# Optimization experiments

Measured on AMD Instinct MI355X. Metric: run time of the kernel, lower is better.

## Reference

```python
import jax, jax.numpy as jnp
import numpy as np

D_MODEL = 512
D_PROJ = 32
N_CENT = 6
CORR_HIDDEN = max(D_MODEL // 16, 32)  # 32
LN_EPS = 1e-5
ALPHA_DIR = 5.0


def _layernorm(x, g, b):
    mu = x.mean(axis=-1, keepdims=True)
    var = jnp.mean((x - mu) ** 2, axis=-1, keepdims=True)
    return (x - mu) * jax.lax.rsqrt(var + LN_EPS) * g + b


def _l2norm(x, eps=1e-12):
    n = jnp.sqrt(jnp.sum(x * x, axis=-1, keepdims=True))
    return x / jnp.maximum(n, eps)


def setup_inputs() -> dict:
    key = jax.random.key(0)
    ks = jax.random.split(key, 8)
    B, N = 64, 1024
    x = jax.random.normal(ks[0], (B, N, D_MODEL), dtype=jnp.float32)
    s_in = 1.0 / np.sqrt(D_MODEL)
    proj_w = jax.random.uniform(ks[1], (D_PROJ, D_MODEL), jnp.float32, -s_in, s_in)
    proj_b = jax.random.uniform(ks[2], (D_PROJ,), jnp.float32, -s_in, s_in)
    ln_g = jnp.ones((D_PROJ,), jnp.float32)
    ln_b = jnp.zeros((D_PROJ,), jnp.float32)
    centroids = jax.random.uniform(ks[3], (N_CENT, D_PROJ), jnp.float32, -3.0, 3.0)
    s_c = 1.0 / np.sqrt(D_MODEL + D_PROJ)
    corr_in_w = jax.random.uniform(ks[4], (CORR_HIDDEN, D_MODEL + D_PROJ), jnp.float32, -s_c, s_c)
    corr_in_b = jax.random.uniform(ks[5], (CORR_HIDDEN,), jnp.float32, -s_c, s_c)
    # correction_out is zero-init in the module; use small random values so the
    # correction path is numerically exercised by the baseline.
    corr_out_w = jax.random.normal(ks[6], (D_MODEL, CORR_HIDDEN), jnp.float32) * 0.02
    corr_out_b = jax.random.normal(ks[7], (D_MODEL,), jnp.float32) * 0.02
    return {
        "x": x, "proj_w": proj_w, "proj_b": proj_b, "ln_g": ln_g, "ln_b": ln_b,
        "centroids": centroids,
        "corr_in_w": corr_in_w, "corr_in_b": corr_in_b,
        "corr_out_w": corr_out_w, "corr_out_b": corr_out_b,
        "gate_alpha": jnp.float32(0.0),
        "routing_log_temp": jnp.float32(1.6),
        "scale_evidence": jnp.float32(5.0),
    }


def reference(x, proj_w, proj_b, ln_g, ln_b, centroids, corr_in_w, corr_in_b,
              corr_out_w, corr_out_b, gate_alpha, routing_log_temp, scale_evidence):
    B, N, D = x.shape
    # per-variate RevIN-style normalization over the variate axis (dim=1), unbiased std
    rev_mean = x.mean(axis=1, keepdims=True)
    rev_var = jnp.sum((x - rev_mean) ** 2, axis=1, keepdims=True) / (N - 1)
    rev_std = jnp.sqrt(rev_var) + 1e-5
    x_norm = (x - rev_mean) / rev_std
    # geometric routing: proj -> LN -> cosine sim against centroids
    Q = _layernorm(jnp.einsum("bnd,pd->bnp", x_norm, proj_w) + proj_b, ln_g, ln_b)
    Q_n = _l2norm(Q)                      # [B,N,P]
    K_n = _l2norm(centroids)              # [K,P]
    sim_cos = jnp.einsum("bnp,kp->bnk", Q_n, K_n)
    soft_assign = jax.nn.softmax(sim_cos * jnp.exp(routing_log_temp), axis=-1)
    centroid_ctx = jnp.einsum("bnk,kp->bnp", soft_assign, centroids)
    # centroid-conditioned correction MLP (dropout is identity in eval)
    corr_input = jnp.concatenate([x_norm, centroid_ctx], axis=-1)  # [B,N,D+P]
    h = jax.nn.gelu(jnp.einsum("bnc,hc->bnh", corr_input, corr_in_w) + corr_in_b, approximate=False)
    correction = (jnp.einsum("bnh,dh->bnd", h, corr_out_w) + corr_out_b) * rev_std
    gate = jax.nn.sigmoid(gate_alpha)
    out = x + gate * correction
    # DST uncertainty (no-grad diagnostic)
    sim_ctrl = jax.lax.stop_gradient(sim_cos)
    dir_gate = jax.nn.softplus((sim_ctrl - sim_ctrl.mean(axis=-1, keepdims=True)) * ALPHA_DIR)
    s_ev = jax.nn.softplus(jax.lax.stop_gradient(scale_evidence))
    S_train = jnp.sum(dir_gate * s_ev + 1.0, axis=-1, keepdims=True)
    u_std = N_CENT / S_train
    # losses
    gram = K_n @ K_n.T
    ortho_loss = jnp.mean((gram - jnp.eye(N_CENT, dtype=x.dtype)) ** 2)
    avg_routing = soft_assign.mean(axis=(0, 1))
    latent_loss = jnp.mean((avg_routing - 1.0 / N_CENT) ** 2)
    return out, u_std, ortho_loss, latent_loss
```

## Files before the change

### kernel.cpp

```cpp
#include <hip/hip_runtime.h>
#include <cstdint>
#include <cstddef>

#define N_DIM 1024
#define D_DIM 512
#define M_DIM 65536
#define NC 6

typedef float f32x4 __attribute__((ext_vector_type(4)));
typedef __bf16 bf16x8 __attribute__((ext_vector_type(8)));

__device__ __forceinline__ float sp_f(float z) {
    return z > 20.f ? z : log1pf(expf(z));
}

__global__ void k_pack(const float* __restrict__ pw, const float* __restrict__ ciw,
                       const float* __restrict__ cow, const float* __restrict__ cent,
                       const float* __restrict__ ga, const float* __restrict__ rlt,
                       const float* __restrict__ sev,
                       __bf16* __restrict__ bpa, __bf16* __restrict__ bpl,
                       __bf16* __restrict__ w3p,
                       float* __restrict__ kn, float* __restrict__ cw,
                       float* __restrict__ scal, float* __restrict__ out_ortho) {
    __shared__ float skn[NC * 32];
    __shared__ float ssq[36];
    int bid = blockIdx.x, tid = threadIdx.x;
    if (bid < 128) {
        int i = bid * 256 + tid;
        int c = i >> 9, k = i & 511;
        float w = (c < 32) ? pw[c * 512 + k] : ciw[(c - 32) * 544 + k];
        __bf16 hi = (__bf16)w;
        bpa[i] = hi;
        if (c < 32) bpl[i] = (__bf16)(w - (float)hi);
    } else if (bid < 192) {
        int j = (bid - 128) * 256 + tid;
        w3p[j] = (__bf16)cow[j];
    } else if (bid == 192) {
        if (tid < 192) {
            int k = tid >> 5, h = tid & 31;
            float s = 0.f;
            for (int p = 0; p < 32; ++p) s += cent[k * 32 + p] * ciw[h * 544 + 512 + p];
            cw[k * 32 + h] = s;
        } else if (tid < 192 + NC) {
            int k = tid - 192;
            float s = 0.f;
            for (int p = 0; p < 32; ++p) { float v = cent[k * 32 + p]; s += v * v; }
            float inv = 1.f / fmaxf(sqrtf(s), 1e-12f);
            for (int p = 0; p < 32; ++p) kn[k * 32 + p] = cent[k * 32 + p] * inv;
        } else if (tid == 198) {
            scal[0] = expf(rlt[0]);
            scal[1] = sp_f(sev[0]);
            scal[2] = 1.f / (1.f + expf(-ga[0]));
        }
    } else {
        if (tid < NC) {
            float s = 0.f;
            for (int p = 0; p < 32; ++p) { float v = cent[tid * 32 + p]; s += v * v; }
            float inv = 1.f / fmaxf(sqrtf(s), 1e-12f);
            for (int p = 0; p < 32; ++p) skn[tid * 32 + p] = cent[tid * 32 + p] * inv;
        }
        __syncthreads();
        if (tid < 36) {
            int i = tid / 6, j = tid % 6;
            float g = 0.f;
            for (int p = 0; p < 32; ++p) g += skn[i * 32 + p] * skn[j * 32 + p];
            float d = g - (i == j ? 1.f : 0.f);
            ssq[tid] = d * d;
        }
        __syncthreads();
        if (tid == 0) {
            float s = 0.f;
            for (int i = 0; i < 36; ++i) s += ssq[i];
            *out_ortho = s / 36.f;
        }
    }
}

__global__ void k_stat1(const float* __restrict__ x, float* __restrict__ part) {
    int bid = blockIdx.x;
    int b = bid >> 5, sub = bid & 31;
    int d4 = threadIdx.x * 4;
    const float* px = x + ((size_t)(b * 1024 + sub * 32)) * 512 + d4;
    f32x4 s = {0.f, 0.f, 0.f, 0.f}, q = s;
    #pragma unroll 8
    for (int i = 0; i < 32; ++i) {
        float4 v = *(const float4*)(px + (size_t)i * 512);
        s.x += v.x; s.y += v.y; s.z += v.z; s.w += v.w;
        q.x += v.x * v.x; q.y += v.y * v.y; q.z += v.z * v.z; q.w += v.w * v.w;
    }
    *(f32x4*)(part + (size_t)bid * 512 + d4) = s;
    *(f32x4*)(part + (size_t)(2048 + bid) * 512 + d4) = q;
}

__global__ void k_stat2(const float* __restrict__ part, float* __restrict__ mean,
                        float* __restrict__ istd, float* __restrict__ stdv) {
    int b = blockIdx.x, d = threadIdx.x;
    float s = 0.f, q = 0.f;
    for (int c = 0; c < 32; ++c) {
        s += part[(size_t)(b * 32 + c) * 512 + d];
        q += part[(size_t)(2048 + b * 32 + c) * 512 + d];
    }
    float mu = s * (1.f / (float)N_DIM);
    float var = fmaxf((q - s * mu) * (1.f / (float)(N_DIM - 1)), 0.f);
    float sd = sqrtf(var) + 1e-5f;
    mean[b * D_DIM + d] = mu;
    istd[b * D_DIM + d] = 1.f / sd;
    stdv[b * D_DIM + d] = sd;
}

__launch_bounds__(256)
__global__ void mega(const float* __restrict__ x,
                     const float* __restrict__ proj_b, const float* __restrict__ ln_g,
                     const float* __restrict__ ln_b, const float* __restrict__ cib,
                     const float* __restrict__ cob,
                     const float* __restrict__ mean, const float* __restrict__ istd,
                     const float* __restrict__ stdv,
                     const float* __restrict__ kn, const float* __restrict__ cw,
                     const float* __restrict__ scal,
                     const __bf16* __restrict__ bpa, const __bf16* __restrict__ bpl,
                     const __bf16* __restrict__ w3p,
                     float* __restrict__ out, float* __restrict__ ustd_out,
                     float* __restrict__ rout_part) {
    __shared__ float s_mean[512];
    __shared__ float s_is[512];
    __shared__ float s_sd[512];
    __shared__ float s_cob[512];
    __shared__ __align__(16) float s_t[3][16][68];
    __shared__ __align__(16) __bf16 s_h[16][40];

    int tid = threadIdx.x;
    int wv = tid >> 6, ln = tid & 63;
    int l15 = ln & 15, lg = ln >> 4;

    int b = blockIdx.x >> 6;
    int wrow = blockIdx.x * 16;

    if (tid < 128) {
        *(float4*)&s_mean[tid * 4] = *(const float4*)(mean + b * 512 + tid * 4);
        *(float4*)&s_sd[tid * 4]   = *(const float4*)(stdv + b * 512 + tid * 4);
    } else {
        int t = tid - 128;
        *(float4*)&s_is[t * 4]  = *(const float4*)(istd + b * 512 + t * 4);
        *(float4*)&s_cob[t * 4] = *(const float4*)(cob + t * 4);
    }
    __syncthreads();

    int kbase = wv * 128;
    const float* xr = x + (size_t)(wrow + l15) * 512 + kbase;
    const __bf16* w0  = bpa + (size_t)l15 * 512 + kbase;
    const __bf16* w1  = bpa + (size_t)(16 + l15) * 512 + kbase;
    const __bf16* w2  = bpa + (size_t)(32 + l15) * 512 + kbase;
    const __bf16* w3  = bpa + (size_t)(48 + l15) * 512 + kbase;
    const __bf16* wl0 = bpl + (size_t)l15 * 512 + kbase;
    const __bf16* wl1 = bpl + (size_t)(16 + l15) * 512 + kbase;

    f32x4 a0 = {0.f, 0.f, 0.f, 0.f}, a1 = a0, a2 = a0, a3 = a0;
    #pragma unroll
    for (int ks = 0; ks < 4; ++ks) {
        int k0 = ks * 32 + lg * 8;
        int kk = kbase + k0;
        float4 xa = *(const float4*)(xr + k0);
        float4 xb = *(const float4*)(xr + k0 + 4);
        float4 ma = *(const float4*)&s_mean[kk];
        float4 m2 = *(const float4*)&s_mean[kk + 4];
        float4 ia = *(const float4*)&s_is[kk];
        float4 i2 = *(const float4*)&s_is[kk + 4];
        float xnf[8];
        xnf[0] = (xa.x - ma.x) * ia.x; xnf[1] = (xa.y - ma.y) * ia.y;
        xnf[2] = (xa.z - ma.z) * ia.z; xnf[3] = (xa.w - ma.w) * ia.w;
        xnf[4] = (xb.x - m2.x) * i2.x; xnf[5] = (xb.y - m2.y) * i2.y;
        xnf[6] = (xb.z - m2.z) * i2.z; xnf[7] = (xb.w - m2.w) * i2.w;
        bf16x8 ah, al;
        #pragma unroll
        for (int j = 0; j < 8; ++j) {
            __bf16 hh = (__bf16)xnf[j];
            ah[j] = hh;
            al[j] = (__bf16)(xnf[j] - (float)hh);
        }
        bf16x8 wh0 = *(const bf16x8*)(w0 + k0);
        bf16x8 wh1 = *(const bf16x8*)(w1 + k0);
        a0 = __builtin_amdgcn_mfma_f32_16x16x32_bf16(ah, wh0, a0, 0, 0, 0);
        a0 = __builtin_amdgcn_mfma_f32_16x16x32_bf16(ah, *(const bf16x8*)(wl0 + k0), a0, 0, 0, 0);
        a0 = __builtin_amdgcn_mfma_f32_16x16x32_bf16(al, wh0, a0, 0, 0, 0);
        a1 = __builtin_amdgcn_mfma_f32_16x16x32_bf16(ah, wh1, a1, 0, 0, 0);
        a1 = __builtin_amdgcn_mfma_f32_16x16x32_bf16(ah, *(const bf16x8*)(wl1 + k0), a1, 0, 0, 0);
        a1 = __builtin_amdgcn_mfma_f32_16x16x32_bf16(al, wh1, a1, 0, 0, 0);
        a2 = __builtin_amdgcn_mfma_f32_16x16x32_bf16(ah, *(const bf16x8*)(w2 + k0), a2, 0, 0, 0);
        a3 = __builtin_amdgcn_mfma_f32_16x16x32_bf16(ah, *(const bf16x8*)(w3 + k0), a3, 0, 0, 0);
    }

    if (wv != 0) {
        int j = wv - 1;
        #pragma unroll
        for (int rg = 0; rg < 4; ++rg) {
            int row = lg * 4 + rg;
            s_t[j][row][l15]      = a0[rg];
            s_t[j][row][16 + l15] = a1[rg];
            s_t[j][row][32 + l15] = a2[rg];
            s_t[j][row][48 + l15] = a3[rg];
        }
    }
    __syncthreads();

    if (wv == 0) {
        #pragma unroll
        for (int rg = 0; rg < 4; ++rg) {
            int row = lg * 4 + rg;
            a0[rg] += s_t[0][row][l15]      + s_t[1][row][l15]      + s_t[2][row][l15];
            a1[rg] += s_t[0][row][16 + l15] + s_t[1][row][16 + l15] + s_t[2][row][16 + l15];
            a2[rg] += s_t[0][row][32 + l15] + s_t[1][row][32 + l15] + s_t[2][row][32 + l15];
            a3[rg] += s_t[0][row][48 + l15] + s_t[1][row][48 + l15] + s_t[2][row][48 + l15];
            s_t[0][row][l15]      = a0[rg];
            s_t[0][row][16 + l15] = a1[rg];
            s_t[0][row][32 + l15] = a2[rg];
            s_t[0][row][48 + l15] = a3[rg];
        }

        int r = ln >> 2, sub = ln & 3;
        const float* tr = &s_t[0][r][0];
        float4 t0 = *(const float4*)(tr + sub * 8);
        float4 t1 = *(const float4*)(tr + sub * 8 + 4);
        float4 pb0 = *(const float4*)(proj_b + sub * 8);
        float4 pb1 = *(const float4*)(proj_b + sub * 8 + 4);
        float P[8];
        P[0] = t0.x + pb0.x; P[1] = t0.y + pb0.y; P[2] = t0.z + pb0.z; P[3] = t0.w + pb0.w;
        P[4] = t1.x + pb1.x; P[5] = t1.y + pb1.y; P[6] = t1.z + pb1.z; P[7] = t1.w + pb1.w;
        float m = 0.f;
        #pragma unroll
        for (int j = 0; j < 8; ++j) m += P[j];
        m += __shfl_xor(m, 1); m += __shfl_xor(m, 2);
        float mu = m * (1.f / 32.f);
        float v = 0.f;
        #pragma unroll
        for (int j = 0; j < 8; ++j) { float d = P[j] - mu; v += d * d; }
        v += __shfl_xor(v, 1); v += __shfl_xor(v, 2);
        float rs = rsqrtf(v * (1.f / 32.f) + 1e-5f);
        float4 g0 = *(const float4*)(ln_g + sub * 8);
        float4 g1 = *(const float4*)(ln_g + sub * 8 + 4);
        float4 bl0 = *(const float4*)(ln_b + sub * 8);
        float4 bl1 = *(const float4*)(ln_b + sub * 8 + 4);
        float gg[8] = {g0.x, g0.y, g0.z, g0.w, g1.x, g1.y, g1.z, g1.w};
        float bb[8] = {bl0.x, bl0.y, bl0.z, bl0.w, bl1.x, bl1.y, bl1.z, bl1.w};
        float q[8]; float n2 = 0.f;
        #pragma unroll
        for (int j = 0; j < 8; ++j) {
            q[j] = (P[j] - mu) * rs * gg[j] + bb[j];
            n2 += q[j] * q[j];
        }
        n2 += __shfl_xor(n2, 1); n2 += __shfl_xor(n2, 2);
        float inv = 1.f / fmaxf(sqrtf(n2), 1e-12f);
        float sim[6];
        #pragma unroll
        for (int k = 0; k < 6; ++k) {
            const float* kr = kn + k * 32 + sub * 8;
            float4 ka = *(const float4*)(kr);
            float4 kb = *(const float4*)(kr + 4);
            float s = q[0] * ka.x + q[1] * ka.y + q[2] * ka.z + q[3] * ka.w
                    + q[4] * kb.x + q[5] * kb.y + q[6] * kb.z + q[7] * kb.w;
            s += __shfl_xor(s, 1); s += __shfl_xor(s, 2);
            sim[k] = s * inv;
        }
        float T = scal[0], sevv = scal[1];
        float mx = sim[0];
        #pragma unroll
        for (int k = 1; k < 6; ++k) mx = fmaxf(mx, sim[k]);
        float e[6], es = 0.f;
        #pragma unroll
        for (int k = 0; k < 6; ++k) { e[k] = expf((sim[k] - mx) * T); es += e[k]; }
        float einv = 1.f / es;
        float a[6];
        #pragma unroll
        for (int k = 0; k < 6; ++k) a[k] = e[k] * einv;
        float msim = 0.f;
        #pragma unroll
        for (int k = 0; k < 6; ++k) msim += sim[k];
        msim *= (1.f / 6.f);
        float S = 6.f;
        #pragma unroll
        for (int k = 0; k < 6; ++k) S += sevv * sp_f((sim[k] - msim) * 5.f);
        if (sub == 0) ustd_out[wrow + r] = 6.f / S;
        float4 h0 = *(const float4*)(tr + 32 + sub * 8);
        float4 h1 = *(const float4*)(tr + 32 + sub * 8 + 4);
        float4 c0 = *(const float4*)(cib + sub * 8);
        float4 c1 = *(const float4*)(cib + sub * 8 + 4);
        float vh[8] = {h0.x + c0.x, h0.y + c0.y, h0.z + c0.z, h0.w + c0.w,
                       h1.x + c1.x, h1.y + c1.y, h1.z + c1.z, h1.w + c1.w};
        #pragma unroll
        for (int k = 0; k < 6; ++k) {
            const float* cr = cw + k * 32 + sub * 8;
            float4 ca = *(const float4*)(cr);
            float4 cb = *(const float4*)(cr + 4);
            vh[0] += a[k] * ca.x; vh[1] += a[k] * ca.y; vh[2] += a[k] * ca.z; vh[3] += a[k] * ca.w;
            vh[4] += a[k] * cb.x; vh[5] += a[k] * cb.y; vh[6] += a[k] * cb.z; vh[7] += a[k] * cb.w;
        }
        bf16x8 hv;
        #pragma unroll
        for (int j = 0; j < 8; ++j) {
            float gv = 0.5f * vh[j] * (1.f + erff(vh[j] * 0.70710678118654752f));
            hv[j] = (__bf16)gv;
        }
        *(bf16x8*)(&s_h[r][sub * 8]) = hv;
        #pragma unroll
        for (int k = 0; k < 6; ++k) {
            float rv = (sub == 0) ? a[k] : 0.f;
            rv += __shfl_xor(rv, 4); rv += __shfl_xor(rv, 8);
            rv += __shfl_xor(rv, 16); rv += __shfl_xor(rv, 32);
            if (ln == 0) atomicAdd(rout_part + (blockIdx.x & 63) * 6 + k, rv);
        }
    }
    __syncthreads();

    bf16x8 ha = *(const bf16x8*)(&s_h[l15][lg * 8]);
    float gate = scal[2];
    int row = wrow + l15;
    const float* xrow = x + (size_t)row * 512;
    float* orow = out + (size_t)row * 512;
    #pragma unroll
    for (int i = 0; i < 8; ++i) {
        int nf = wv * 8 + i;
        int col = nf * 16 + l15;
        bf16x8 wb = *(const bf16x8*)(w3p + col * 32 + lg * 8);
        f32x4 z = {0.f, 0.f, 0.f, 0.f};
        f32x4 d = __builtin_amdgcn_mfma_f32_16x16x32_bf16(wb, ha, z, 0, 0, 0);
        int colb = nf * 16 + lg * 4;
        float4 xv = *(const float4*)(xrow + colb);
        float4 bi = *(const float4*)&s_cob[colb];
        float4 sd = *(const float4*)&s_sd[colb];
        f32x4 o;
        o[0] = xv.x + gate * ((d[0] + bi.x) * sd.x);
        o[1] = xv.y + gate * ((d[1] + bi.y) * sd.y);
        o[2] = xv.z + gate * ((d[2] + bi.z) * sd.z);
        o[3] = xv.w + gate * ((d[3] + bi.w) * sd.w);
        *(f32x4*)(orow + colb) = o;
    }
}

__global__ void k5(const float* __restrict__ rp, float* __restrict__ out_latent) {
    __shared__ float sv[6];
    int t = threadIdx.x;
    if (t < 6) {
        float s = 0.f;
        for (int i = 0; i < 64; ++i) s += rp[i * 6 + t];
        sv[t] = s;
    }
    __syncthreads();
    if (t == 0) {
        float s = 0.f;
        for (int k = 0; k < 6; ++k) {
            float av = sv[k] * (1.f / (float)M_DIM) - (1.f / 6.f);
            s += av * av;
        }
        *out_latent = s / 6.f;
    }
}

extern "C" void kernel_launch(void* const* d_in, const int* in_sizes, int n_in,
                              void* d_out, int out_size, void* d_ws, size_t ws_size,
                              hipStream_t stream) {
    const float* x      = (const float*)d_in[0];
    const float* proj_w = (const float*)d_in[1];
    const float* proj_b = (const float*)d_in[2];
    const float* ln_g   = (const float*)d_in[3];
    const float* ln_b   = (const float*)d_in[4];
    const float* cent   = (const float*)d_in[5];
    const float* ciw    = (const float*)d_in[6];
    const float* cib    = (const float*)d_in[7];
    const float* cow    = (const float*)d_in[8];
    const float* cob    = (const float*)d_in[9];
    const float* ga     = (const float*)d_in[10];
    const float* rlt    = (const float*)d_in[11];
    const float* sev    = (const float*)d_in[12];

    char* ws = (char*)d_ws;
    float*  rout = (float*)(ws + 0);
    float*  kn   = (float*)(ws + 2048);
    float*  cwv  = (float*)(ws + 4096);
    float*  scal = (float*)(ws + 6144);
    __bf16* bpa  = (__bf16*)(ws + 8192);
    __bf16* bpl  = (__bf16*)(ws + 73728);
    __bf16* w3p  = (__bf16*)(ws + 106496);
    float*  mean = (float*)(ws + 139264);
    float*  istd = (float*)(ws + 270336);
    float*  stdv = (float*)(ws + 401408);

    float* outp   = (float*)d_out;
    float* ustd   = outp + (size_t)M_DIM * D_DIM;
    float* ortho  = ustd + M_DIM;
    float* latent = ortho + 1;

    float* part = (float*)d_out;

    hipMemsetAsync(rout, 0, 64 * 6 * sizeof(float), stream);
    k_pack<<<194, 256, 0, stream>>>(proj_w, ciw, cow, cent, ga, rlt, sev,
                                    bpa, bpl, w3p, kn, cwv, scal, ortho);
    k_stat1<<<2048, 128, 0, stream>>>(x, part);
    k_stat2<<<64, 512, 0, stream>>>(part, mean, istd, stdv);
    mega<<<4096, 256, 0, stream>>>(x, proj_b, ln_g, ln_b, cib, cob,
                                   mean, istd, stdv, kn, cwv, scal,
                                   bpa, bpl, w3p, outp, ustd, rout);
    k5<<<1, 64, 0, stream>>>(rout, latent);
}
```

Before: 146.4 us.

## Stage x tile in LDS with coalesced loads/stores and atomic partial-sum reduction

Loads each block's 16x512 fp32 x tile once from global memory with fully coalesced float4 reads into shared memory. Both the projection GEMM and the final residual read x from LDS, which removes the second global read of x. The output is written back to LDS and then stored coalesced. Cross-wave partial sums are now reduced with LDS atomicAdd instead of a three-buffer staging step. In exchange, LDS use grows by about 33KB per block, which may lower occupancy, and the float atomics change the summation order.

```diff
diff --git a/kernel.cpp b/kernel.cpp
--- a/kernel.cpp
+++ b/kernel.cpp
@@ -125,7 +125,8 @@
     __shared__ float s_is[512];
     __shared__ float s_sd[512];
     __shared__ float s_cob[512];
-    __shared__ __align__(16) float s_t[3][16][68];
+    __shared__ __align__(16) float s_xio[16][516];
+    __shared__ __align__(16) float s_acc[16][68];
     __shared__ __align__(16) __bf16 s_h[16][40];
 
     int tid = threadIdx.x;
@@ -134,6 +135,11 @@
 
     int b = blockIdx.x >> 6;
     int wrow = blockIdx.x * 16;
+
+    const float* xsrc = x + (size_t)wrow * 512;
+    f32x4 tv[8];
+    #pragma unroll
+    for (int j = 0; j < 8; ++j) tv[j] = *(const f32x4*)(xsrc + j * 1024 + tid * 4);
 
     if (tid < 128) {
         *(float4*)&s_mean[tid * 4] = *(const float4*)(mean + b * 512 + tid * 4);
@@ -143,10 +149,16 @@
         *(float4*)&s_is[t * 4]  = *(const float4*)(istd + b * 512 + t * 4);
         *(float4*)&s_cob[t * 4] = *(const float4*)(cob + t * 4);
     }
+    #pragma unroll
+    for (int i = tid; i < 16 * 68; i += 256) ((float*)s_acc)[i] = 0.f;
+    #pragma unroll
+    for (int j = 0; j < 8; ++j) {
+        int flat = j * 1024 + tid * 4;
+        *(f32x4*)&s_xio[flat >> 9][flat & 511] = tv[j];
+    }
     __syncthreads();
 
     int kbase = wv * 128;
-    const float* xr = x + (size_t)(wrow + l15) * 512 + kbase;
     const __bf16* w0  = bpa + (size_t)l15 * 512 + kbase;
     const __bf16* w1  = bpa + (size_t)(16 + l15) * 512 + kbase;
     const __bf16* w2  = bpa + (size_t)(32 + l15) * 512 + kbase;
@@ -159,17 +171,17 @@
     for (int ks = 0; ks < 4; ++ks) {
         int k0 = ks * 32 + lg * 8;
         int kk = kbase + k0;
-        float4 xa = *(const float4*)(xr + k0);
-        float4 xb = *(const float4*)(xr + k0 + 4);
+        f32x4 xa = *(const f32x4*)&s_xio[l15][kk];
+        f32x4 xb = *(const f32x4*)&s_xio[l15][kk + 4];
         float4 ma = *(const float4*)&s_mean[kk];
         float4 m2 = *(const float4*)&s_mean[kk + 4];
         float4 ia = *(const float4*)&s_is[kk];
         float4 i2 = *(const float4*)&s_is[kk + 4];
         float xnf[8];
-        xnf[0] = (xa.x - ma.x) * ia.x; xnf[1] = (xa.y - ma.y) * ia.y;
-        xnf[2] = (xa.z - ma.z) * ia.z; xnf[3] = (xa.w - ma.w) * ia.w;
-        xnf[4] = (xb.x - m2.x) * i2.x; xnf[5] = (xb.y - m2.y) * i2.y;
-        xnf[6] = (xb.z - m2.z) * i2.z; xnf[7] = (xb.w - m2.w) * i2.w;
+        xnf[0] = (xa[0] - ma.x) * ia.x; xnf[1] = (xa[1] - ma.y) * ia.y;
+        xnf[2] = (xa[2] - ma.z) * ia.z; xnf[3] = (xa[3] - ma.w) * ia.w;
+        xnf[4] = (xb[0] - m2.x) * i2.x; xnf[5] = (xb[1] - m2.y) * i2.y;
+        xnf[6] = (xb[2] - m2.z) * i2.z; xnf[7] = (xb[3] - m2.w) * i2.w;
         bf16x8 ah, al;
         #pragma unroll
         for (int j = 0; j < 8; ++j) {
@@ -189,35 +201,19 @@
         a3 = __builtin_amdgcn_mfma_f32_16x16x32_bf16(ah, *(const bf16x8*)(w3 + k0), a3, 0, 0, 0);
     }
 
-    if (wv != 0) {
-        int j = wv - 1;
-        #pragma unroll
-        for (int rg = 0; rg < 4; ++rg) {
-            int row = lg * 4 + rg;
-            s_t[j][row][l15]      = a0[rg];
-            s_t[j][row][16 + l15] = a1[rg];
-            s_t[j][row][32 + l15] = a2[rg];
-            s_t[j][row][48 + l15] = a3[rg];
-        }
+    #pragma unroll
+    for (int rg = 0; rg < 4; ++rg) {
+        int row = lg * 4 + rg;
+        atomicAdd(&s_acc[row][l15],      a0[rg]);
+        atomicAdd(&s_acc[row][16 + l15], a1[rg]);
+        atomicAdd(&s_acc[row][32 + l15], a2[rg]);
+        atomicAdd(&s_acc[row][48 + l15], a3[rg]);
     }
     __syncthreads();
 
     if (wv == 0) {
-        #pragma unroll
-        for (int rg = 0; rg < 4; ++rg) {
-            int row = lg * 4 + rg;
-            a0[rg] += s_t[0][row][l15]      + s_t[1][row][l15]      + s_t[2][row][l15];
-            a1[rg] += s_t[0][row][16 + l15] + s_t[1][row][16 + l15] + s_t[2][row][16 + l15];
-            a2[rg] += s_t[0][row][32 + l15] + s_t[1][row][32 + l15] + s_t[2][row][32 + l15];
-            a3[rg] += s_t[0][row][48 + l15] + s_t[1][row][48 + l15] + s_t[2][row][48 + l15];
-            s_t[0][row][l15]      = a0[rg];
-            s_t[0][row][16 + l15] = a1[rg];
-            s_t[0][row][32 + l15] = a2[rg];
-            s_t[0][row][48 + l15] = a3[rg];
-        }
-
         int r = ln >> 2, sub = ln & 3;
-        const float* tr = &s_t[0][r][0];
+        const float* tr = &s_acc[r][0];
         float4 t0 = *(const float4*)(tr + sub * 8);
         float4 t1 = *(const float4*)(tr + sub * 8 + 4);
         float4 pb0 = *(const float4*)(proj_b + sub * 8);
@@ -312,9 +308,6 @@
 
     bf16x8 ha = *(const bf16x8*)(&s_h[l15][lg * 8]);
     float gate = scal[2];
-    int row = wrow + l15;
-    const float* xrow = x + (size_t)row * 512;
-    float* orow = out + (size_t)row * 512;
     #pragma unroll
     for (int i = 0; i < 8; ++i) {
         int nf = wv * 8 + i;
@@ -323,15 +316,28 @@
         f32x4 z = {0.f, 0.f, 0.f, 0.f};
         f32x4 d = __builtin_amdgcn_mfma_f32_16x16x32_bf16(wb, ha, z, 0, 0, 0);
         int colb = nf * 16 + lg * 4;
-        float4 xv = *(const float4*)(xrow + colb);
+        f32x4 xv = *(const f32x4*)&s_xio[l15][colb];
         float4 bi = *(const float4*)&s_cob[colb];
         float4 sd = *(const float4*)&s_sd[colb];
         f32x4 o;
-        o[0] = xv.x + gate * ((d[0] + bi.x) * sd.x);
-        o[1] = xv.y + gate * ((d[1] + bi.y) * sd.y);
-        o[2] = xv.z + gate * ((d[2] + bi.z) * sd.z);
-        o[3] = xv.w + gate * ((d[3] + bi.w) * sd.w);
-        *(f32x4*)(orow + colb) = o;
+        o[0] = xv[0] + gate * ((d[0] + bi.x) * sd.x);
+        o[1] = xv[1] + gate * ((d[1] + bi.y) * sd.y);
+        o[2] = xv[2] + gate * ((d[2] + bi.z) * sd.z);
+        o[3] = xv[3] + gate * ((d[3] + bi.w) * sd.w);
+        *(f32x4*)&s_xio[l15][colb] = o;
+    }
+    __syncthreads();
+
+    float* odst = out + (size_t)wrow * 512;
+    f32x4 ov[8];
+    #pragma unroll
+    for (int j = 0; j < 8; ++j) {
+        int flat = j * 1024 + tid * 4;
+        ov[j] = *(const f32x4*)&s_xio[flat >> 9][flat & 511];
+    }
+    #pragma unroll
+    for (int j = 0; j < 8; ++j) {
+        *(f32x4*)(odst + j * 1024 + tid * 4) = ov[j];
     }
 }
 
```

Result: slower. 203.4 us (+38.9%).

## Give each wave its own rows over full K and drop block barriers

Applied to the files above, without the earlier changes.

Replaces the split-K scheme, where four waves each reduced a quarter of K over the same 16 rows and merged through LDS with barriers. Each wave now owns 16 rows and loops over all of K, so the LDS reduction and both __syncthreads are gone. The per-row LayerNorm, routing and GELU work moves from wave 0 alone to all four waves, and the grid shrinks to 1024 blocks. mean, istd, stdv and the output bias are now read from global memory instead of being staged in LDS, and the epilogue prefetches the next group of x and weight loads in software. The trade-off is longer serial chains per wave, fewer blocks in flight, and more register pressure from the prefetch buffers.

```diff
diff --git a/kernel.cpp b/kernel.cpp
--- a/kernel.cpp
+++ b/kernel.cpp
@@ -121,50 +121,38 @@
                      const __bf16* __restrict__ w3p,
                      float* __restrict__ out, float* __restrict__ ustd_out,
                      float* __restrict__ rout_part) {
-    __shared__ float s_mean[512];
-    __shared__ float s_is[512];
-    __shared__ float s_sd[512];
-    __shared__ float s_cob[512];
-    __shared__ __align__(16) float s_t[3][16][68];
-    __shared__ __align__(16) __bf16 s_h[16][40];
+    __shared__ __align__(16) float s_tile[4][16][68];
+    __shared__ __align__(16) __bf16 s_h[4][16][40];
 
     int tid = threadIdx.x;
     int wv = tid >> 6, ln = tid & 63;
     int l15 = ln & 15, lg = ln >> 4;
 
-    int b = blockIdx.x >> 6;
-    int wrow = blockIdx.x * 16;
-
-    if (tid < 128) {
-        *(float4*)&s_mean[tid * 4] = *(const float4*)(mean + b * 512 + tid * 4);
-        *(float4*)&s_sd[tid * 4]   = *(const float4*)(stdv + b * 512 + tid * 4);
-    } else {
-        int t = tid - 128;
-        *(float4*)&s_is[t * 4]  = *(const float4*)(istd + b * 512 + t * 4);
-        *(float4*)&s_cob[t * 4] = *(const float4*)(cob + t * 4);
-    }
-    __syncthreads();
-
-    int kbase = wv * 128;
-    const float* xr = x + (size_t)(wrow + l15) * 512 + kbase;
-    const __bf16* w0  = bpa + (size_t)l15 * 512 + kbase;
-    const __bf16* w1  = bpa + (size_t)(16 + l15) * 512 + kbase;
-    const __bf16* w2  = bpa + (size_t)(32 + l15) * 512 + kbase;
-    const __bf16* w3  = bpa + (size_t)(48 + l15) * 512 + kbase;
-    const __bf16* wl0 = bpl + (size_t)l15 * 512 + kbase;
-    const __bf16* wl1 = bpl + (size_t)(16 + l15) * 512 + kbase;
+    int row0 = blockIdx.x * 64;
+    int b = row0 >> 10;
+    int wrow = row0 + wv * 16;
+
+    const float* xr = x + (size_t)(wrow + l15) * 512;
+    const float* mb = mean + b * 512;
+    const float* ib = istd + b * 512;
+
+    const __bf16* w0  = bpa + (size_t)l15 * 512;
+    const __bf16* w1  = bpa + (size_t)(16 + l15) * 512;
+    const __bf16* w2  = bpa + (size_t)(32 + l15) * 512;
+    const __bf16* w3  = bpa + (size_t)(48 + l15) * 512;
+    const __bf16* wl0 = bpl + (size_t)l15 * 512;
+    const __bf16* wl1 = bpl + (size_t)(16 + l15) * 512;
 
     f32x4 a0 = {0.f, 0.f, 0.f, 0.f}, a1 = a0, a2 = a0, a3 = a0;
-    #pragma unroll
-    for (int ks = 0; ks < 4; ++ks) {
+    #pragma unroll 4
+    for (int ks = 0; ks < 16; ++ks) {
         int k0 = ks * 32 + lg * 8;
-        int kk = kbase + k0;
         float4 xa = *(const float4*)(xr + k0);
         float4 xb = *(const float4*)(xr + k0 + 4);
-        float4 ma = *(const float4*)&s_mean[kk];
-        float4 m2 = *(const float4*)&s_mean[kk + 4];
-        float4 ia = *(const float4*)&s_is[kk];
-        float4 i2 = *(const float4*)&s_is[kk + 4];
+        float4 ma = *(const float4*)(mb + k0);
+        float4 m2 = *(const float4*)(mb + k0 + 4);
+        float4 ia = *(const float4*)(ib + k0);
+        float4 i2 = *(const float4*)(ib + k0 + 4);
         float xnf[8];
         xnf[0] = (xa.x - ma.x) * ia.x; xnf[1] = (xa.y - ma.y) * ia.y;
         xnf[2] = (xa.z - ma.z) * ia.z; xnf[3] = (xa.w - ma.w) * ia.w;
@@ -188,36 +176,18 @@
         a2 = __builtin_amdgcn_mfma_f32_16x16x32_bf16(ah, *(const bf16x8*)(w2 + k0), a2, 0, 0, 0);
         a3 = __builtin_amdgcn_mfma_f32_16x16x32_bf16(ah, *(const bf16x8*)(w3 + k0), a3, 0, 0, 0);
     }
-
-    if (wv != 0) {
-        int j = wv - 1;
-        #pragma unroll
-        for (int rg = 0; rg < 4; ++rg) {
-            int row = lg * 4 + rg;
-            s_t[j][row][l15]      = a0[rg];
-            s_t[j][row][16 + l15] = a1[rg];
-            s_t[j][row][32 + l15] = a2[rg];
-            s_t[j][row][48 + l15] = a3[rg];
-        }
-    }
-    __syncthreads();
-
-    if (wv == 0) {
-        #pragma unroll
-        for (int rg = 0; rg < 4; ++rg) {
-            int row = lg * 4 + rg;
-            a0[rg] += s_t[0][row][l15]      + s_t[1][row][l15]      + s_t[2][row][l15];
-            a1[rg] += s_t[0][row][16 + l15] + s_t[1][row][16 + l15] + s_t[2][row][16 + l15];
-            a2[rg] += s_t[0][row][32 + l15] + s_t[1][row][32 + l15] + s_t[2][row][32 + l15];
-            a3[rg] += s_t[0][row][48 + l15] + s_t[1][row][48 + l15] + s_t[2][row][48 + l15];
-            s_t[0][row][l15]      = a0[rg];
-            s_t[0][row][16 + l15] = a1[rg];
-            s_t[0][row][32 + l15] = a2[rg];
-            s_t[0][row][48 + l15] = a3[rg];
-        }
-
+    #pragma unroll
+    for (int rg = 0; rg < 4; ++rg) {
+        int row = lg * 4 + rg;
+        s_tile[wv][row][l15]      = a0[rg];
+        s_tile[wv][row][16 + l15] = a1[rg];
+        s_tile[wv][row][32 + l15] = a2[rg];
+        s_tile[wv][row][48 + l15] = a3[rg];
+    }
+
+    {
         int r = ln >> 2, sub = ln & 3;
-        const float* tr = &s_t[0][r][0];
+        const float* tr = &s_tile[wv][r][0];
         float4 t0 = *(const float4*)(tr + sub * 8);
         float4 t1 = *(const float4*)(tr + sub * 8 + 4);
         float4 pb0 = *(const float4*)(proj_b + sub * 8);
@@ -299,7 +269,7 @@
             float gv = 0.5f * vh[j] * (1.f + erff(vh[j] * 0.70710678118654752f));
             hv[j] = (__bf16)gv;
         }
-        *(bf16x8*)(&s_h[r][sub * 8]) = hv;
+        *(bf16x8*)(&s_h[wv][r][sub * 8]) = hv;
         #pragma unroll
         for (int k = 0; k < 6; ++k) {
             float rv = (sub == 0) ? a[k] : 0.f;
@@ -308,30 +278,53 @@
             if (ln == 0) atomicAdd(rout_part + (blockIdx.x & 63) * 6 + k, rv);
         }
     }
-    __syncthreads();
-
-    bf16x8 ha = *(const bf16x8*)(&s_h[l15][lg * 8]);
+
+    bf16x8 ha = *(const bf16x8*)(&s_h[wv][l15][lg * 8]);
     float gate = scal[2];
     int row = wrow + l15;
     const float* xrow = x + (size_t)row * 512;
     float* orow = out + (size_t)row * 512;
+    const float* sb = stdv + b * 512;
+
+    f32x4 xB[4]; bf16x8 wB[4]; float4 biB[4]; float4 sdB[4];
     #pragma unroll
-    for (int i = 0; i < 8; ++i) {
-        int nf = wv * 8 + i;
-        int col = nf * 16 + l15;
-        bf16x8 wb = *(const bf16x8*)(w3p + col * 32 + lg * 8);
-        f32x4 z = {0.f, 0.f, 0.f, 0.f};
-        f32x4 d = __builtin_amdgcn_mfma_f32_16x16x32_bf16(wb, ha, z, 0, 0, 0);
-        int colb = nf * 16 + lg * 4;
-        float4 xv = *(const float4*)(xrow + colb);
-        float4 bi = *(const float4*)&s_cob[colb];
-        float4 sd = *(const float4*)&s_sd[colb];
-        f32x4 o;
-        o[0] = xv.x + gate * ((d[0] + bi.x) * sd.x);
-        o[1] = xv.y + gate * ((d[1] + bi.y) * sd.y);
-        o[2] = xv.z + gate * ((d[2] + bi.z) * sd.z);
-        o[3] = xv.w + gate * ((d[3] + bi.w) * sd.w);
-        *(f32x4*)(orow + colb) = o;
+    for (int i = 0; i < 4; ++i) {
+        int nf = i;
+        xB[i]  = *(const f32x4*)(xrow + nf * 16 + lg * 4);
+        wB[i]  = *(const bf16x8*)(w3p + (nf * 16 + l15) * 32 + lg * 8);
+        biB[i] = *(const float4*)(cob + nf * 16 + lg * 4);
+        sdB[i] = *(const float4*)(sb + nf * 16 + lg * 4);
+    }
+    #pragma unroll
+    for (int c = 0; c < 8; ++c) {
+        f32x4 xN[4]; bf16x8 wN[4]; float4 biN[4]; float4 sdN[4];
+        if (c < 7) {
+            #pragma unroll
+            for (int i = 0; i < 4; ++i) {
+                int nf = (c + 1) * 4 + i;
+                xN[i]  = *(const f32x4*)(xrow + nf * 16 + lg * 4);
+                wN[i]  = *(const bf16x8*)(w3p + (nf * 16 + l15) * 32 + lg * 8);
+                biN[i] = *(const float4*)(cob + nf * 16 + lg * 4);
+                sdN[i] = *(const float4*)(sb + nf * 16 + lg * 4);
+            }
+        }
+        #pragma unroll
+        for (int i = 0; i < 4; ++i) {
+            int nf = c * 4 + i;
+            f32x4 z = {0.f, 0.f, 0.f, 0.f};
+            f32x4 d = __builtin_amdgcn_mfma_f32_16x16x32_bf16(wB[i], ha, z, 0, 0, 0);
+            int colb = nf * 16 + lg * 4;
+            f32x4 o;
+            o[0] = xB[i][0] + gate * ((d[0] + biB[i].x) * sdB[i].x);
+            o[1] = xB[i][1] + gate * ((d[1] + biB[i].y) * sdB[i].y);
+            o[2] = xB[i][2] + gate * ((d[2] + biB[i].z) * sdB[i].z);
+            o[3] = xB[i][3] + gate * ((d[3] + biB[i].w) * sdB[i].w);
+            *(f32x4*)(orow + colb) = o;
+        }
+        if (c < 7) {
+            #pragma unroll
+            for (int i = 0; i < 4; ++i) { xB[i] = xN[i]; wB[i] = wN[i]; biB[i] = biN[i]; sdB[i] = sdN[i]; }
+        }
     }
 }
 
@@ -395,7 +388,7 @@
                                     bpa, bpl, w3p, kn, cwv, scal, ortho);
     k_stat1<<<2048, 128, 0, stream>>>(x, part);
     k_stat2<<<64, 512, 0, stream>>>(part, mean, istd, stdv);
-    mega<<<4096, 256, 0, stream>>>(x, proj_b, ln_g, ln_b, cib, cob,
+    mega<<<1024, 256, 0, stream>>>(x, proj_b, ln_g, ln_b, cib, cob,
                                    mean, istd, stdv, kn, cwv, scal,
                                    bpa, bpl, w3p, outp, ustd, rout);
     k5<<<1, 64, 0, stream>>>(rout, latent);
```

Measured after the change: 156.7 us. 1.07x slower.
